# Performance work log

Hardware: AMD Instinct MI355X
Metric: run time of the kernel (lower is better)

## Reference

```python
import jax, jax.numpy as jnp
import numpy as np

B, S, HID = 2, 2048, 2560
H, HKV, D = 8, 4, 256          # query heads, kv heads, head_dim
GROUPS = H // HKV
Q_SIZE, KV_SIZE = H * D, HKV * D
SLIDING_WINDOW = 512
SCALE = 256.0 ** -0.5          # query_pre_attn_scalar ** -0.5
EPS = 1e-6
ROPE_THETA = 10000.0


def setup_inputs() -> dict:
    key = jax.random.key(0)
    k1, k2, k3 = jax.random.split(key, 3)
    return {
        "hidden_states": jax.random.normal(k1, (B, S, HID), jnp.float32),
        "w_qkv": jax.random.normal(k2, (HID, Q_SIZE + 2 * KV_SIZE), jnp.float32) * (HID ** -0.5),
        "w_o": jax.random.normal(k3, (H * D, HID), jnp.float32) * ((H * D) ** -0.5),
        "q_norm_w": jnp.zeros((D,), jnp.float32),   # Gemma RMSNorm uses (1 + w)
        "k_norm_w": jnp.zeros((D,), jnp.float32),
        "positions": jnp.arange(S, dtype=jnp.int32),
    }


def _gemma_rms_norm(x, w, eps=EPS):
    # Gemma3RMSNorm: normalize in fp32, scale by (1 + w)
    xf = x.astype(jnp.float32)
    n = xf * jax.lax.rsqrt(jnp.mean(xf * xf, axis=-1, keepdims=True) + eps)
    return (n * (1.0 + w)).astype(x.dtype)


def _rope(q, k, positions):
    # q: [B,S,H,D], k: [B,S,HKV,D]; rotate_half RoPE, unsqueeze_dim=2 (head axis)
    half = D // 2
    inv_freq = 1.0 / (ROPE_THETA ** (jnp.arange(0, D, 2, dtype=jnp.float32) / D))  # [D/2]
    ang = positions.astype(jnp.float32)[:, None] * inv_freq[None, :]               # [S,D/2]
    emb = jnp.concatenate([ang, ang], axis=-1)                                     # [S,D]
    cos = jnp.cos(emb)[None, :, None, :]
    sin = jnp.sin(emb)[None, :, None, :]

    def rot(x):
        x1, x2 = x[..., :half], x[..., half:]
        return jnp.concatenate([-x2, x1], axis=-1)

    return q * cos + rot(q) * sin, k * cos + rot(k) * sin


def reference(hidden_states, w_qkv, w_o, q_norm_w, k_norm_w, positions):
    bsz, q_len, _ = hidden_states.shape
    qkv = jnp.einsum("bsh,hd->bsd", hidden_states, w_qkv)
    q, k, v = jnp.split(qkv, [Q_SIZE, Q_SIZE + KV_SIZE], axis=-1)
    Q = q.reshape(bsz, q_len, H, D)
    K = k.reshape(bsz, q_len, HKV, D)
    V = v.reshape(bsz, q_len, HKV, D)

    Q = _gemma_rms_norm(Q, q_norm_w)
    K = _gemma_rms_norm(K, k_norm_w)
    Q, K = _rope(Q, K, positions)

    # GQA: repeat kv heads to match query heads
    Kr = jnp.repeat(K, GROUPS, axis=2)  # [B,S,H,D]
    Vr = jnp.repeat(V, GROUPS, axis=2)

    scores = jnp.einsum("bqhd,bkhd->bhqk", Q, Kr) * SCALE  # [B,H,S,S]

    i = positions[:, None].astype(jnp.int32)
    j = positions[None, :].astype(jnp.int32)
    mask = (j <= i) & ((i - j) < SLIDING_WINDOW)           # causal + sliding window
    scores = jnp.where(mask[None, None, :, :], scores, jnp.float32(-1e30))

    probs = jax.nn.softmax(scores.astype(jnp.float32), axis=-1).astype(Q.dtype)
    out = jnp.einsum("bhqk,bkhd->bqhd", probs, Vr).reshape(bsz, q_len, H * D)
    return jnp.einsum("bsd,dh->bsh", out, w_o)
```

## Files before the change

### kernel.cpp

```cpp
#include <hip/hip_runtime.h>
#include <hip/hip_bf16.h>
#include <stdint.h>

#define QSCALE 0.09016844005555459f

typedef __attribute__((ext_vector_type(4))) float f32x4;
typedef __attribute__((ext_vector_type(8))) __bf16 bf16x8;
typedef __attribute__((ext_vector_type(8))) unsigned short ushort8;

static __device__ __forceinline__ float bf2f(unsigned short v) {
  union { unsigned u; float f; } x; x.u = ((unsigned)v) << 16; return x.f;
}
static __device__ __forceinline__ unsigned short f2bf(float f) {
  union { float f; unsigned u; } x; x.f = f;
  unsigned r = x.u + 0x7fffu + ((x.u >> 16) & 1u);
  return (unsigned short)(r >> 16);
}
static __device__ __forceinline__ void gload16(const void* g, void* l) {
  __builtin_amdgcn_global_load_lds((const __attribute__((address_space(1))) void*)g,
                                   (__attribute__((address_space(3))) void*)l, 16, 0, 0);
}
#define SBAR() __builtin_amdgcn_s_barrier()
#define SCHEDB() __builtin_amdgcn_sched_barrier(0)

__global__ __launch_bounds__(256) void k_rope_tab(const int* __restrict__ pos,
                                                  float* __restrict__ ct,
                                                  float* __restrict__ st) {
  int idx = blockIdx.x * 256 + threadIdx.x;
  int s = idx >> 7, j = idx & 127;
  float inv = exp2f((float)j * (-13.287712379549449f / 128.0f));
  float ang = (float)pos[s] * inv;
  float sv, cv;
  sincosf(ang, &sv, &cv);
  ct[idx] = cv; st[idx] = sv;
}

__global__ __launch_bounds__(256) void k_cvt_bf16(const float* __restrict__ in,
                                                  unsigned short* __restrict__ out, int n4) {
  int i = blockIdx.x * 256 + threadIdx.x;
  if (i >= n4) return;
  float4 v = ((const float4*)in)[i];
  ushort4 o; o.x = f2bf(v.x); o.y = f2bf(v.y); o.z = f2bf(v.z); o.w = f2bf(v.w);
  ((ushort4*)out)[i] = o;
}

__global__ __launch_bounds__(256) void k_transpose_w(const float* __restrict__ in,
                                                     unsigned short* __restrict__ out,
                                                     int R, int C) {
  __shared__ float tile[32][33];
  int c0 = blockIdx.x * 32, r0 = blockIdx.y * 32;
  int tx = threadIdx.x & 31, ty = threadIdx.x >> 5;
#pragma unroll
  for (int i = 0; i < 4; i++)
    tile[ty + 8*i][tx] = in[(size_t)(r0 + ty + 8*i) * C + c0 + tx];
  __syncthreads();
#pragma unroll
  for (int i = 0; i < 4; i++)
    out[(size_t)(c0 + ty + 8*i) * R + r0 + tx] = f2bf(tile[tx][ty + 8*i]);
}

template <bool F32OUT>
__global__ __launch_bounds__(512, 1) void k_gemm256(const unsigned short* __restrict__ A,
                                                    const unsigned short* __restrict__ Bt,
                                                    void* __restrict__ Cm,
                                                    int M, int N, int K) {
  __shared__ __align__(16) unsigned short ldsA[4][8192];
  __shared__ __align__(16) unsigned short ldsB[4][8192];
  const int nbn = N >> 8;
  int bid = blockIdx.x;
  int nwg = gridDim.x;
  if ((nwg & 7) == 0) {
    int cpx = nwg >> 3;
    bid = (bid & 7) * cpx + (bid >> 3);
  }
  const int bm = bid / nbn, bn = bid % nbn;
  const int tid = threadIdx.x;
  const int w = tid >> 6, l = tid & 63;
  const int wm = w >> 2, wn = w & 3;
  const int lr = l & 15, lk = l >> 4;
  const int nt = K >> 5;

  const int rL = tid >> 2;
  const int swc = ((tid & 3) ^ ((tid >> 3) & 3)) << 3;
  const unsigned short* Ag = A + (size_t)(bm * 256 + rL) * K + swc;
  const unsigned short* Bg = Bt + (size_t)(bn * 256 + rL) * K + swc;
  const int ldsoff = w * 512;
  const int wb = ((lk ^ ((lr >> 1) & 3)) << 3);
  const int arow0 = wm * 128 + lr;
  const int brow0 = wn * 64 + lr;

  f32x4 acc[8][4] = {};

#define STAGE_A(kt_) do { int s_ = (kt_) & 3; \
    gload16(Ag + (size_t)(kt_) * 32,                    (char*)&ldsA[s_][ldsoff]); \
    gload16(Ag + (size_t)(kt_) * 32 + (size_t)128 * K,  (char*)&ldsA[s_][4096 + ldsoff]); } while (0)
#define STAGE_B(kt_) do { int s_ = (kt_) & 3; \
    gload16(Bg + (size_t)(kt_) * 32,                    (char*)&ldsB[s_][ldsoff]); \
    gload16(Bg + (size_t)(kt_) * 32 + (size_t)128 * K,  (char*)&ldsB[s_][4096 + ldsoff]); } while (0)

  STAGE_A(0); STAGE_B(0);
  if (nt > 1) { STAGE_A(1); STAGE_B(1); }
  if (nt > 2) { STAGE_A(2); STAGE_B(2); }
  if (nt > 2) { asm volatile("s_waitcnt vmcnt(8)" ::: "memory"); }
  else        { asm volatile("s_waitcnt vmcnt(0)" ::: "memory"); }
  SCHEDB();
  SBAR();

  for (int kt = 0; kt < nt; ++kt) {
    const int s = kt & 3;
    const bool pf = (kt + 3) < nt;
    bf16x8 af[4], bf[4];
#pragma unroll
    for (int i = 0; i < 4; ++i)
      af[i] = *(const bf16x8*)&ldsA[s][((arow0 + i * 16) << 5) + wb];
#pragma unroll
    for (int j = 0; j < 4; ++j)
      bf[j] = *(const bf16x8*)&ldsB[s][((brow0 + j * 16) << 5) + wb];
    if (pf) STAGE_A(kt + 3);
    SBAR();
    __builtin_amdgcn_s_setprio(1);
#pragma unroll
    for (int i = 0; i < 4; ++i)
#pragma unroll
      for (int j = 0; j < 4; ++j)
        acc[i][j] = __builtin_amdgcn_mfma_f32_16x16x32_bf16(af[i], bf[j], acc[i][j], 0, 0, 0);
    __builtin_amdgcn_s_setprio(0);
    SBAR();
#pragma unroll
    for (int i = 0; i < 4; ++i)
      af[i] = *(const bf16x8*)&ldsA[s][((arow0 + (i + 4) * 16) << 5) + wb];
    if (pf) STAGE_B(kt + 3);
    SBAR();
    __builtin_amdgcn_s_setprio(1);
#pragma unroll
    for (int i = 0; i < 4; ++i)
#pragma unroll
      for (int j = 0; j < 4; ++j)
        acc[i + 4][j] = __builtin_amdgcn_mfma_f32_16x16x32_bf16(af[i], bf[j], acc[i + 4][j], 0, 0, 0);
    __builtin_amdgcn_s_setprio(0);
    int ahead = nt - 1 - kt;
    if (ahead >= 1) {
      if (ahead >= 3)      { asm volatile("s_waitcnt vmcnt(8)" ::: "memory"); }
      else if (ahead == 2) { asm volatile("s_waitcnt vmcnt(4)" ::: "memory"); }
      else                 { asm volatile("s_waitcnt vmcnt(0)" ::: "memory"); }
      SCHEDB();
      SBAR();
    }
  }
#undef STAGE_A
#undef STAGE_B

#pragma unroll
  for (int i = 0; i < 8; ++i)
#pragma unroll
    for (int j = 0; j < 4; ++j) {
      int row = bm * 256 + wm * 128 + i * 16 + lk * 4;
      int col = bn * 256 + wn * 64 + j * 16 + lr;
#pragma unroll
      for (int r = 0; r < 4; ++r) {
        if constexpr (F32OUT)
          ((float*)Cm)[(size_t)(row + r) * N + col] = acc[i][j][r];
        else
          ((unsigned short*)Cm)[(size_t)(row + r) * N + col] = f2bf(acc[i][j][r]);
      }
    }
}

__global__ __launch_bounds__(256) void k_norm_rope(
    const unsigned short* __restrict__ qkv,
    const float* __restrict__ qw, const float* __restrict__ kw,
    const float* __restrict__ ct, const float* __restrict__ st,
    unsigned short* __restrict__ Qh, unsigned short* __restrict__ Kh) {
  int gwid = (blockIdx.x * 256 + threadIdx.x) >> 6;
  int l = threadIdx.x & 63;
  int head = gwid % 12;
  int bs = gwid / 12;
  int b = bs >> 11, s = bs & 2047;
  bool isq = head < 8;
  int col = isq ? head * 256 : 2048 + (head - 8) * 256;
  const unsigned short* src = qkv + (size_t)bs * 4096 + col;
  int d0 = l * 4;
  ushort4 u = *(const ushort4*)(src + d0);
  float x0 = bf2f(u.x), x1 = bf2f(u.y), x2 = bf2f(u.z), x3 = bf2f(u.w);
  float ss = x0 * x0 + x1 * x1 + x2 * x2 + x3 * x3;
#pragma unroll
  for (int off = 32; off > 0; off >>= 1) ss += __shfl_xor(ss, off);
  float inv = rsqrtf(ss * (1.0f / 256.0f) + 1e-6f);
  const float* wv = isq ? qw : kw;
  float4 w4 = *(const float4*)(wv + d0);
  float y0 = x0 * inv * (1.0f + w4.x);
  float y1 = x1 * inv * (1.0f + w4.y);
  float y2 = x2 * inv * (1.0f + w4.z);
  float y3 = x3 * inv * (1.0f + w4.w);
  int fb = (l & 31) * 4;
  float4 c4 = *(const float4*)(ct + s * 128 + fb);
  float4 s4 = *(const float4*)(st + s * 128 + fb);
  float p0 = __shfl_xor(y0, 32), p1 = __shfl_xor(y1, 32);
  float p2 = __shfl_xor(y2, 32), p3 = __shfl_xor(y3, 32);
  float sg = (l < 32) ? -1.0f : 1.0f;
  float o0 = y0 * c4.x + sg * p0 * s4.x;
  float o1 = y1 * c4.y + sg * p1 * s4.y;
  float o2 = y2 * c4.z + sg * p2 * s4.z;
  float o3 = y3 * c4.w + sg * p3 * s4.w;
  if (isq) {
    o0 *= QSCALE; o1 *= QSCALE; o2 *= QSCALE; o3 *= QSCALE;
    unsigned short* dst = Qh + (((size_t)(b * 8 + head)) * 2048 + s) * 256 + d0;
    ushort4 o; o.x = f2bf(o0); o.y = f2bf(o1); o.z = f2bf(o2); o.w = f2bf(o3);
    *(ushort4*)dst = o;
  } else {
    int hk = head - 8;
    int ch = d0 >> 3;
    int dsw = ((ch ^ (s & 7)) << 3) | (d0 & 7);
    unsigned short* dst = Kh + (((size_t)(b * 4 + hk)) * 2048 + s) * 256 + dsw;
    ushort4 o; o.x = f2bf(o0); o.y = f2bf(o1); o.z = f2bf(o2); o.w = f2bf(o3);
    *(ushort4*)dst = o;
  }
}

__global__ __launch_bounds__(256) void k_vtrans(const unsigned short* __restrict__ qkv,
                                                unsigned short* __restrict__ VT) {
  __shared__ __align__(16) unsigned short tile[64][72];
  int bid = blockIdx.x;
  int dt = bid & 3, stile = (bid >> 2) & 31, hk = (bid >> 7) & 3, b = bid >> 9;
  int s0 = stile * 64, d0 = dt * 64;
  int t = threadIdx.x;
#pragma unroll
  for (int i = 0; i < 2; i++) {
    int flat = i * 256 + t;
    int sl = flat >> 3, dc = flat & 7;
    ushort8 v = *(const ushort8*)&qkv[(size_t)(b * 2048 + s0 + sl) * 4096 + 3072 + hk * 256 + d0 + dc * 8];
    *(ushort8*)&tile[sl][dc * 8] = v;
  }
  __syncthreads();
#pragma unroll
  for (int i = 0; i < 2; i++) {
    int flat = i * 256 + t;
    int dl = flat >> 3, sc = flat & 7;
    ushort8 v;
#pragma unroll
    for (int j = 0; j < 8; j++) v[j] = tile[sc * 8 + j][dl];
    int dg = d0 + dl;
    int chg = (s0 >> 3) + sc;
    int swc = chg ^ (dg & 7);
    *(ushort8*)&VT[((size_t)(b * 4 + hk) * 256 + dg) * 2048 + swc * 8] = v;
  }
}

__global__ __launch_bounds__(256) void k_attn(
    const unsigned short* __restrict__ Qh,
    const unsigned short* __restrict__ Kh,
    const unsigned short* __restrict__ VT,
    const int* __restrict__ pos,
    unsigned short* __restrict__ Ao) {
  __shared__ __align__(16) unsigned short Ks[64 * 256];
  __shared__ __align__(16) unsigned short Vs[256 * 64];
  __shared__ __align__(16) unsigned short Ps[4][16 * 72];
  int bid = blockIdx.x;
  int qt = bid & 31, h = (bid >> 5) & 7, b = bid >> 8;
  int hk = h >> 1;
  int t = threadIdx.x, w = t >> 6, l = t & 63;
  int lr = l & 15, lk = l >> 4;
  int q0 = qt * 64, qrow0 = q0 + w * 16;
  const unsigned short* qbase = Qh + (((size_t)(b * 8 + h)) * 2048 + (qrow0 + lr)) * 256;
  bf16x8 qf[8];
#pragma unroll
  for (int c = 0; c < 8; c++) qf[c] = *(const bf16x8*)&qbase[c * 32 + lk * 8];
  int pq[4];
#pragma unroll
  for (int r = 0; r < 4; r++) pq[r] = pos[qrow0 + lk * 4 + r];
  float m[4], ll[4];
  f32x4 oacc[16];
  f32x4 zero4 = {0.f, 0.f, 0.f, 0.f};
#pragma unroll
  for (int r = 0; r < 4; r++) { m[r] = -1e30f; ll[r] = 0.0f; }
#pragma unroll
  for (int nd = 0; nd < 16; nd++) oacc[nd] = zero4;
  const char* Kbase = (const char*)(Kh + ((size_t)(b * 4 + hk)) * 2048 * 256);
  const char* Vbase = (const char*)(VT + ((size_t)(b * 4 + hk)) * 256 * 2048);
  int jlo = q0 - 511; if (jlo < 0) jlo = 0; jlo &= ~63;
  for (int j0 = jlo; j0 < q0 + 64; j0 += 64) {
#pragma unroll
    for (int i = 0; i < 8; i++)
      gload16(Kbase + (size_t)j0 * 512 + i * 4096 + t * 16, (char*)Ks + i * 4096 + w * 1024);
#pragma unroll
    for (int i = 0; i < 8; i++) {
      int off = i * 4096 + t * 16;
      int d = off >> 7, rb = off & 127;
      gload16(Vbase + (size_t)d * 4096 + j0 * 2 + rb, (char*)Vs + i * 4096 + w * 1024);
    }
    __syncthreads();
    f32x4 sacc[4];
#pragma unroll
    for (int n = 0; n < 4; n++) sacc[n] = zero4;
#pragma unroll
    for (int n = 0; n < 4; n++) {
      int key = n * 16 + lr;
      int sw = (key & 7) << 4;
#pragma unroll
      for (int c = 0; c < 8; c++) {
        bf16x8 kf = *(const bf16x8*)((const char*)Ks + key * 512 + ((c * 64 + lk * 16) ^ sw));
        sacc[n] = __builtin_amdgcn_mfma_f32_16x16x32_bf16(qf[c], kf, sacc[n], 0, 0, 0);
      }
    }
    int pk[4];
#pragma unroll
    for (int n = 0; n < 4; n++) pk[n] = pos[j0 + n * 16 + lr];
#pragma unroll
    for (int n = 0; n < 4; n++)
#pragma unroll
      for (int r = 0; r < 4; r++) {
        int dq = pq[r] - pk[n];
        if (!(dq >= 0 && dq < 512)) sacc[n][r] = -1e30f;
      }
    float tm[4], rs[4], mn[4], corr[4];
#pragma unroll
    for (int r = 0; r < 4; r++)
      tm[r] = fmaxf(fmaxf(sacc[0][r], sacc[1][r]), fmaxf(sacc[2][r], sacc[3][r]));
#pragma unroll
    for (int d = 1; d < 16; d <<= 1)
#pragma unroll
      for (int r = 0; r < 4; r++) tm[r] = fmaxf(tm[r], __shfl_xor(tm[r], d));
#pragma unroll
    for (int r = 0; r < 4; r++) {
      mn[r] = fmaxf(m[r], tm[r]);
      corr[r] = exp2f(m[r] - mn[r]);
      rs[r] = 0.f;
    }
#pragma unroll
    for (int n = 0; n < 4; n++)
#pragma unroll
      for (int r = 0; r < 4; r++) {
        float sv = sacc[n][r];
        float p = (sv > -1e29f) ? exp2f(sv - mn[r]) : 0.0f;
        sacc[n][r] = p;
        rs[r] += p;
      }
#pragma unroll
    for (int d = 1; d < 16; d <<= 1)
#pragma unroll
      for (int r = 0; r < 4; r++) rs[r] += __shfl_xor(rs[r], d);
#pragma unroll
    for (int r = 0; r < 4; r++) { ll[r] = ll[r] * corr[r] + rs[r]; m[r] = mn[r]; }
#pragma unroll
    for (int nd = 0; nd < 16; nd++)
#pragma unroll
      for (int r = 0; r < 4; r++) oacc[nd][r] *= corr[r];
#pragma unroll
    for (int n = 0; n < 4; n++)
#pragma unroll
      for (int r = 0; r < 4; r++)
        Ps[w][(lk * 4 + r) * 72 + n * 16 + lr] = f2bf(sacc[n][r]);
#pragma unroll
    for (int c2 = 0; c2 < 2; c2++) {
      bf16x8 pf = *(const bf16x8*)&Ps[w][lr * 72 + c2 * 32 + lk * 8];
#pragma unroll
      for (int nd = 0; nd < 16; nd++) {
        int dr = nd * 16 + lr;
        bf16x8 vf = *(const bf16x8*)((const char*)Vs + dr * 128 + ((c2 * 64 + lk * 16) ^ ((dr & 7) << 4)));
        oacc[nd] = __builtin_amdgcn_mfma_f32_16x16x32_bf16(pf, vf, oacc[nd], 0, 0, 0);
      }
    }
    __syncthreads();
  }
#pragma unroll
  for (int r = 0; r < 4; r++) ll[r] = 1.0f / ll[r];
#pragma unroll
  for (int nd = 0; nd < 16; nd++)
#pragma unroll
    for (int r = 0; r < 4; r++) {
      float v = oacc[nd][r] * ll[r];
      Ao[((size_t)(b * 2048 + qrow0 + lk * 4 + r)) * 2048 + h * 256 + nd * 16 + lr] = f2bf(v);
    }
}

extern "C" void kernel_launch(void* const* d_in, const int* in_sizes, int n_in,
                              void* d_out, int out_size, void* d_ws, size_t ws_size,
                              hipStream_t stream) {
  const float* hs   = (const float*)d_in[0];
  const float* wqkv = (const float*)d_in[1];
  const float* wo   = (const float*)d_in[2];
  const float* qnw  = (const float*)d_in[3];
  const float* knw  = (const float*)d_in[4];
  const int*   pos  = (const int*)d_in[5];
  float* out = (float*)d_out;

  char* base = (char*)d_ws;
  const size_t OFF_R0 = 0;
  const size_t OFF_R1 = 33554432;
  const size_t OFF_R2 = 54525952;
  const size_t OFF_R3 = 75497472;

  unsigned short* QKV = (unsigned short*)(base + OFF_R0);
  unsigned short* Ao  = (unsigned short*)(base + OFF_R0);
  unsigned short* WoT = (unsigned short*)(base + OFF_R0 + 16777216);
  unsigned short* Xb  = (unsigned short*)(base + OFF_R1);
  unsigned short* Qh  = (unsigned short*)(base + OFF_R1);
  unsigned short* WqT = (unsigned short*)(base + OFF_R2);
  unsigned short* Kh  = (unsigned short*)(base + OFF_R2);
  unsigned short* VT  = (unsigned short*)(base + OFF_R2 + 8388608);
  float* ct = (float*)(base + OFF_R3);
  float* st = (float*)(base + OFF_R3 + 1048576);

  k_rope_tab<<<1024, 256, 0, stream>>>(pos, ct, st);
  k_cvt_bf16<<<10240, 256, 0, stream>>>(hs, Xb, 2621440);
  k_transpose_w<<<dim3(128, 80), 256, 0, stream>>>(wqkv, WqT, 2560, 4096);
  k_gemm256<false><<<256, 512, 0, stream>>>(Xb, WqT, QKV, 4096, 4096, 2560);
  k_norm_rope<<<12288, 256, 0, stream>>>(QKV, qnw, knw, ct, st, Qh, Kh);
  k_vtrans<<<1024, 256, 0, stream>>>(QKV, VT);
  k_transpose_w<<<dim3(80, 64), 256, 0, stream>>>(wo, WoT, 2048, 2560);
  k_attn<<<512, 256, 0, stream>>>(Qh, Kh, VT, pos, Ao);
  k_gemm256<true><<<160, 512, 0, stream>>>(Ao, WoT, out, 4096, 2560, 2048);
}
```

Baseline: 265.8 us.

## Shrink GEMM tiles to 256x128 with double-buffered pipeline and higher occupancy

The GEMM kernel now uses 256x128 output tiles instead of 256x256, with 8 waves laid out 4x2, a 2-stage LDS double buffer instead of 4 stages, and launch bounds allowing more blocks per CU. Grid sizes double (512 and 320 blocks), which improves CU fill on a 256-CU part. The cost is lower data reuse per tile, a simpler prefetch that waits for all loads every iteration (vmcnt(0)), and less latency hiding within a single block.

```diff
diff --git a/kernel.cpp b/kernel.cpp
--- a/kernel.cpp
+++ b/kernel.cpp
@@ -21,7 +21,6 @@
                                    (__attribute__((address_space(3))) void*)l, 16, 0, 0);
 }
 #define SBAR() __builtin_amdgcn_s_barrier()
-#define SCHEDB() __builtin_amdgcn_sched_barrier(0)
 
 __global__ __launch_bounds__(256) void k_rope_tab(const int* __restrict__ pos,
                                                   float* __restrict__ ct,
@@ -60,13 +59,13 @@
 }
 
 template <bool F32OUT>
-__global__ __launch_bounds__(512, 1) void k_gemm256(const unsigned short* __restrict__ A,
-                                                    const unsigned short* __restrict__ Bt,
-                                                    void* __restrict__ Cm,
-                                                    int M, int N, int K) {
-  __shared__ __align__(16) unsigned short ldsA[4][8192];
-  __shared__ __align__(16) unsigned short ldsB[4][8192];
-  const int nbn = N >> 8;
+__global__ __launch_bounds__(512, 4) void k_gemm256x128(const unsigned short* __restrict__ A,
+                                                        const unsigned short* __restrict__ Bt,
+                                                        void* __restrict__ Cm,
+                                                        int M, int N, int K) {
+  __shared__ __align__(16) unsigned short ldsA[2][8192];
+  __shared__ __align__(16) unsigned short ldsB[2][4096];
+  const int nbn = N >> 7;
   int bid = blockIdx.x;
   int nwg = gridDim.x;
   if ((nwg & 7) == 0) {
@@ -76,39 +75,33 @@
   const int bm = bid / nbn, bn = bid % nbn;
   const int tid = threadIdx.x;
   const int w = tid >> 6, l = tid & 63;
-  const int wm = w >> 2, wn = w & 3;
+  const int wm = w >> 1, wn = w & 1;
   const int lr = l & 15, lk = l >> 4;
   const int nt = K >> 5;
 
-  const int rL = tid >> 2;
-  const int swc = ((tid & 3) ^ ((tid >> 3) & 3)) << 3;
-  const unsigned short* Ag = A + (size_t)(bm * 256 + rL) * K + swc;
-  const unsigned short* Bg = Bt + (size_t)(bn * 256 + rL) * K + swc;
-  const int ldsoff = w * 512;
+  const int rA0 = tid >> 2, chk = tid & 3;
+  const unsigned short* Ag0 = A + (size_t)(bm * 256 + rA0) * K + ((chk ^ ((rA0 >> 1) & 3)) << 3);
+  const int rA1 = 128 + rA0;
+  const unsigned short* Ag1 = A + (size_t)(bm * 256 + rA1) * K + ((chk ^ ((rA1 >> 1) & 3)) << 3);
+  const unsigned short* Bg0 = Bt + (size_t)(bn * 128 + rA0) * K + ((chk ^ ((rA0 >> 1) & 3)) << 3);
   const int wb = ((lk ^ ((lr >> 1) & 3)) << 3);
-  const int arow0 = wm * 128 + lr;
+  const int arow0 = wm * 64 + lr;
   const int brow0 = wn * 64 + lr;
 
-  f32x4 acc[8][4] = {};
-
-#define STAGE_A(kt_) do { int s_ = (kt_) & 3; \
-    gload16(Ag + (size_t)(kt_) * 32,                    (char*)&ldsA[s_][ldsoff]); \
-    gload16(Ag + (size_t)(kt_) * 32 + (size_t)128 * K,  (char*)&ldsA[s_][4096 + ldsoff]); } while (0)
-#define STAGE_B(kt_) do { int s_ = (kt_) & 3; \
-    gload16(Bg + (size_t)(kt_) * 32,                    (char*)&ldsB[s_][ldsoff]); \
-    gload16(Bg + (size_t)(kt_) * 32 + (size_t)128 * K,  (char*)&ldsB[s_][4096 + ldsoff]); } while (0)
-
-  STAGE_A(0); STAGE_B(0);
-  if (nt > 1) { STAGE_A(1); STAGE_B(1); }
-  if (nt > 2) { STAGE_A(2); STAGE_B(2); }
-  if (nt > 2) { asm volatile("s_waitcnt vmcnt(8)" ::: "memory"); }
-  else        { asm volatile("s_waitcnt vmcnt(0)" ::: "memory"); }
-  SCHEDB();
+  f32x4 acc[4][4] = {};
+
+#define STAGE(kt_) do { int s_ = (kt_) & 1; \
+    gload16(Ag0 + (size_t)(kt_) * 32, (char*)&ldsA[s_][tid * 8]); \
+    gload16(Ag1 + (size_t)(kt_) * 32, (char*)&ldsA[s_][4096 + tid * 8]); \
+    gload16(Bg0 + (size_t)(kt_) * 32, (char*)&ldsB[s_][tid * 8]); } while (0)
+
+  STAGE(0);
+  asm volatile("s_waitcnt vmcnt(0)" ::: "memory");
   SBAR();
 
-  for (int kt = 0; kt < nt; ++kt) {
-    const int s = kt & 3;
-    const bool pf = (kt + 3) < nt;
+  for (int kt = 0; kt < nt - 1; ++kt) {
+    const int s = kt & 1;
+    STAGE(kt + 1);
     bf16x8 af[4], bf[4];
 #pragma unroll
     for (int i = 0; i < 4; ++i)
@@ -116,8 +109,6 @@
 #pragma unroll
     for (int j = 0; j < 4; ++j)
       bf[j] = *(const bf16x8*)&ldsB[s][((brow0 + j * 16) << 5) + wb];
-    if (pf) STAGE_A(kt + 3);
-    SBAR();
     __builtin_amdgcn_s_setprio(1);
 #pragma unroll
     for (int i = 0; i < 4; ++i)
@@ -125,37 +116,32 @@
       for (int j = 0; j < 4; ++j)
         acc[i][j] = __builtin_amdgcn_mfma_f32_16x16x32_bf16(af[i], bf[j], acc[i][j], 0, 0, 0);
     __builtin_amdgcn_s_setprio(0);
+    asm volatile("s_waitcnt vmcnt(0)" ::: "memory");
     SBAR();
+  }
+  {
+    const int s = (nt - 1) & 1;
+    bf16x8 af[4], bf[4];
 #pragma unroll
     for (int i = 0; i < 4; ++i)
-      af[i] = *(const bf16x8*)&ldsA[s][((arow0 + (i + 4) * 16) << 5) + wb];
-    if (pf) STAGE_B(kt + 3);
-    SBAR();
-    __builtin_amdgcn_s_setprio(1);
+      af[i] = *(const bf16x8*)&ldsA[s][((arow0 + i * 16) << 5) + wb];
+#pragma unroll
+    for (int j = 0; j < 4; ++j)
+      bf[j] = *(const bf16x8*)&ldsB[s][((brow0 + j * 16) << 5) + wb];
 #pragma unroll
     for (int i = 0; i < 4; ++i)
 #pragma unroll
       for (int j = 0; j < 4; ++j)
-        acc[i + 4][j] = __builtin_amdgcn_mfma_f32_16x16x32_bf16(af[i], bf[j], acc[i + 4][j], 0, 0, 0);
-    __builtin_amdgcn_s_setprio(0);
-    int ahead = nt - 1 - kt;
-    if (ahead >= 1) {
-      if (ahead >= 3)      { asm volatile("s_waitcnt vmcnt(8)" ::: "memory"); }
-      else if (ahead == 2) { asm volatile("s_waitcnt vmcnt(4)" ::: "memory"); }
-      else                 { asm volatile("s_waitcnt vmcnt(0)" ::: "memory"); }
-      SCHEDB();
-      SBAR();
-    }
-  }
-#undef STAGE_A
-#undef STAGE_B
-
-#pragma unroll
-  for (int i = 0; i < 8; ++i)
+        acc[i][j] = __builtin_amdgcn_mfma_f32_16x16x32_bf16(af[i], bf[j], acc[i][j], 0, 0, 0);
+  }
+#undef STAGE
+
+#pragma unroll
+  for (int i = 0; i < 4; ++i)
 #pragma unroll
     for (int j = 0; j < 4; ++j) {
-      int row = bm * 256 + wm * 128 + i * 16 + lk * 4;
-      int col = bn * 256 + wn * 64 + j * 16 + lr;
+      int row = bm * 256 + wm * 64 + i * 16 + lk * 4;
+      int col = bn * 128 + wn * 64 + j * 16 + lr;
 #pragma unroll
       for (int r = 0; r < 4; ++r) {
         if constexpr (F32OUT)
@@ -404,10 +390,10 @@
   k_rope_tab<<<1024, 256, 0, stream>>>(pos, ct, st);
   k_cvt_bf16<<<10240, 256, 0, stream>>>(hs, Xb, 2621440);
   k_transpose_w<<<dim3(128, 80), 256, 0, stream>>>(wqkv, WqT, 2560, 4096);
-  k_gemm256<false><<<256, 512, 0, stream>>>(Xb, WqT, QKV, 4096, 4096, 2560);
+  k_gemm256x128<false><<<512, 512, 0, stream>>>(Xb, WqT, QKV, 4096, 4096, 2560);
   k_norm_rope<<<12288, 256, 0, stream>>>(QKV, qnw, knw, ct, st, Qh, Kh);
   k_vtrans<<<1024, 256, 0, stream>>>(QKV, VT);
   k_transpose_w<<<dim3(80, 64), 256, 0, stream>>>(wo, WoT, 2048, 2560);
   k_attn<<<512, 256, 0, stream>>>(Qh, Kh, VT, pos, Ao);
-  k_gemm256<true><<<160, 512, 0, stream>>>(Ao, WoT, out, 4096, 2560, 2048);
-}
+  k_gemm256x128<true><<<320, 512, 0, stream>>>(Ao, WoT, out, 4096, 2560, 2048);
+}
```

Result: no change. 265.3 us (-0.2%).
